# Optimization experiments

Hardware: AMD Instinct MI355X
Metric: run time of the kernel (lower is better)

## Reference

```python
import jax, jax.numpy as jnp
import numpy as np

B, NSEQ, SEQ_PER = 2, 4, 256
S = NSEQ * SEQ_PER            # total sequence (stocks interleaved along seq dim)
D, H, HD = 1024, 16, 64       # d_model, nhead, head_dim
HD2, HD4 = HD // 2, HD // 4
DFF = 4096
LAMBDA_INIT = 0.2             # lambda_init_fn(0) = 0.8 - 0.6*exp(0)
SCALING = 1.0 / float(np.sqrt(HD2))
EPS_DEF = float(np.finfo(np.float32).eps)   # torch RMSNorm default eps (eps=None)
EPS_ATTN = 1e-5


def _rms(x, w, eps):
    return x * jax.lax.rsqrt(jnp.mean(x * x, axis=-1, keepdims=True) + eps) * w


def _rope(x, fc):
    # x: (B, T, NSEQ, 2H, HD2); fc: (T, HD4, 2) holding (cos, sin)
    xr = x.reshape(x.shape[:-1] + (HD4, 2))
    c = fc[None, :, None, None, :, 0]
    s = fc[None, :, None, None, :, 1]
    x0, x1 = xr[..., 0], xr[..., 1]
    return jnp.stack([x0 * c - x1 * s, x0 * s + x1 * c], axis=-1).reshape(x.shape)


def setup_inputs():
    key = jax.random.key(0)
    ks = jax.random.split(key, 16)
    def w(i, shape, std=0.02):
        return jax.random.normal(ks[i], shape, jnp.float32) * std
    # true RoPE table for seq_per_stock-1 positions
    t = jnp.arange(SEQ_PER - 1, dtype=jnp.float32)[:, None]
    inv = 1.0 / (10000.0 ** (jnp.arange(HD4, dtype=jnp.float32) / HD4))
    ang = t * inv[None, :]
    return {
        "x": jax.random.normal(ks[0], (B, S, D), jnp.float32),
        "freqs_cis": jnp.stack([jnp.cos(ang), jnp.sin(ang)], axis=-1),
        "w_norm1": jnp.ones((D,), jnp.float32),
        "w_norm2": jnp.ones((D,), jnp.float32),
        "Wq": w(1, (H * HD, D)), "bq": jnp.zeros((H * HD,), jnp.float32),
        "Wk": w(2, (H * HD, D)), "bk": jnp.zeros((H * HD,), jnp.float32),
        "Wv": w(3, (H * HD, D)), "bv": jnp.zeros((H * HD,), jnp.float32),
        "Wo": w(4, (D, H * HD)), "bo": jnp.zeros((D,), jnp.float32),
        "lq1": w(5, (HD2,), 0.1), "lk1": w(6, (HD2,), 0.1),
        "lq2": w(7, (HD2,), 0.1), "lk2": w(8, (HD2,), 0.1),
        "w_attn_norm": jnp.ones((HD,), jnp.float32),
        "Wg": w(9, (2 * DFF, D)), "bg": jnp.zeros((2 * DFF,), jnp.float32),
        "Wout": w(10, (D, DFF)), "bout": jnp.zeros((D,), jnp.float32),
    }


def reference(x, freqs_cis, w_norm1, w_norm2, Wq, bq, Wk, bk, Wv, bv, Wo, bo,
              lq1, lk1, lq2, lk2, w_attn_norm, Wg, bg, Wout, bout):
    Bz, Sz, _ = x.shape
    h = _rms(x, w_norm1, EPS_DEF)
    q = (h @ Wq.T + bq).reshape(Bz, SEQ_PER, NSEQ, 2 * H, HD2)
    k = (h @ Wk.T + bk).reshape(Bz, SEQ_PER, NSEQ, 2 * H, HD2)
    v = (h @ Wv.T + bv).reshape(Bz, Sz, H, HD).transpose(0, 2, 1, 3)   # (B,H,S,HD), interleaved order
    # RoPE on all but the first per-stock timestep; same freqs for every stock
    q = jnp.concatenate([q[:, :1], _rope(q[:, 1:], freqs_cis)], axis=1)
    k = jnp.concatenate([k[:, :1], _rope(k[:, 1:], freqs_cis)], axis=1)
    # reorder q/k to stock-major flat sequence (torch permute(0,4,1,2,3)+reshape)
    q = q.transpose(0, 2, 1, 3, 4).reshape(Bz, Sz, 2 * H, HD2).transpose(0, 2, 1, 3)
    k = k.transpose(0, 2, 1, 3, 4).reshape(Bz, Sz, 2 * H, HD2).transpose(0, 2, 1, 3)
    scores = jnp.einsum('bhqd,bhkd->bhqk', q, k) * SCALING              # (B,2H,S,S)
    causal = jnp.triu(jnp.ones((SEQ_PER, SEQ_PER), bool), 1)
    mask = jnp.tile(causal, (NSEQ, NSEQ))   # block-tiled causal, as torch .repeat
    att = jnp.sign(scores) * jax.nn.softmax(
        jnp.where(mask, -1e30, jnp.abs(scores)), axis=-1)
    lam = jnp.exp(jnp.sum(lk1 * lq1)) - jnp.exp(jnp.sum(lk2 * lq2)) + LAMBDA_INIT
    att = att.reshape(Bz, H, 2, Sz, Sz)
    a1, a2 = att[:, :, 0], att[:, :, 1]
    G = jnp.mean(a1, axis=-2, keepdims=True)          # mean over queries, broadcast back
    a = jnp.where(mask, 0.0, a1 - lam * a2 + lam * G)
    ao = jnp.einsum('bhqk,bhkd->bhqd', a, v)          # v kept in interleaved order (faithful to source)
    ao = _rms(ao, w_attn_norm, EPS_ATTN)
    ao = ao.reshape(Bz, Sz, H * HD)  # flat reinterpret (B,H,S,HD)->(B,S,H*HD), matches torch reshape chain
    x = x + ao @ Wo.T + bo
    h2 = _rms(x, w_norm2, EPS_DEF)
    u, vg = jnp.split(h2 @ Wg.T + bg, 2, axis=-1)
    return x + (u * jax.nn.silu(vg)) @ Wout.T + bout
```

## Files before the change

kernel.cpp:

```cpp
#include <hip/hip_runtime.h>

#define LAMBDA_INIT 0.2f
#define SCALING 0.17677669529663687f
#define EPS_DEF 1.1920928955078125e-07f
#define EPS_ATTN 1e-5f

typedef unsigned short us4 __attribute__((ext_vector_type(4)));
typedef unsigned short us8v __attribute__((ext_vector_type(8)));
typedef float f32x4 __attribute__((ext_vector_type(4)));
typedef float f32x2 __attribute__((ext_vector_type(2)));
typedef __bf16 bf16x8 __attribute__((ext_vector_type(8)));

#define MFMA16(a, b, c) __builtin_amdgcn_mfma_f32_16x16x32_bf16((a), (b), (c), 0, 0, 0)

__device__ __forceinline__ float bf2f(unsigned short u) {
    unsigned int x = ((unsigned int)u) << 16;
    return __builtin_bit_cast(float, x);
}
__device__ __forceinline__ unsigned short f2bf(float f) {
    unsigned int x = __builtin_bit_cast(unsigned int, f);
    x += 0x7fffu + ((x >> 16) & 1u);
    return (unsigned short)(x >> 16);
}
__device__ __forceinline__ void split8(f32x4 a, f32x4 b, us8v& hi, us8v& lo) {
#pragma unroll
    for (int u = 0; u < 4; u++) {
        unsigned short h = f2bf(a[u]);
        hi[u] = h; lo[u] = f2bf(a[u] - bf2f(h));
        unsigned short h2 = f2bf(b[u]);
        hi[4 + u] = h2; lo[4 + u] = f2bf(b[u] - bf2f(h2));
    }
}
__device__ __forceinline__ bf16x8 ldb(const unsigned short* p) {
    return __builtin_bit_cast(bf16x8, *(const us8v*)p);
}

__device__ __forceinline__ float wave_sum(float v) {
#pragma unroll
    for (int o = 32; o > 0; o >>= 1) v += __shfl_down(v, o);
    return v;
}
__device__ __forceinline__ float block_sum(float v, float* red4) {
    int wv = threadIdx.x >> 6;
    float w = wave_sum(v);
    __syncthreads();
    if ((threadIdx.x & 63) == 0) red4[wv] = w;
    __syncthreads();
    return red4[0] + red4[1] + red4[2] + red4[3];
}

__global__ __launch_bounds__(256) void prep(float* __restrict__ G, float* __restrict__ lamp,
                                            const float* lq1, const float* lk1,
                                            const float* lq2, const float* lk2) {
    int i = (blockIdx.x * 256 + threadIdx.x) * 4;
    G[i] = 0.f; G[i + 1] = 0.f; G[i + 2] = 0.f; G[i + 3] = 0.f;
    if (blockIdx.x == 0 && threadIdx.x == 0) {
        float a = 0.f, c = 0.f;
        for (int d = 0; d < 32; d++) {
            a += lq1[d] * lk1[d];
            c += lq2[d] * lk2[d];
        }
        *lamp = expf(a) - expf(c) + LAMBDA_INIT;
    }
}

__global__ __launch_bounds__(256) void cvt_bf16(const float* __restrict__ s,
                                                unsigned short* __restrict__ d, int n4) {
    int i = blockIdx.x * 256 + threadIdx.x;
    if (i >= n4) return;
    f32x4 v = ((const f32x4*)s)[i];
    us4 o;
#pragma unroll
    for (int u = 0; u < 4; u++) o[u] = f2bf(v[u]);
    ((us4*)d)[i] = o;
}

__global__ __launch_bounds__(256) void cvt_split(const float* __restrict__ s,
                                                 unsigned short* __restrict__ hi,
                                                 unsigned short* __restrict__ lo, int n4) {
    int i = blockIdx.x * 256 + threadIdx.x;
    if (i >= n4) return;
    f32x4 v = ((const f32x4*)s)[i];
    us4 h, l;
#pragma unroll
    for (int u = 0; u < 4; u++) {
        h[u] = f2bf(v[u]);
        l[u] = f2bf(v[u] - bf2f(h[u]));
    }
    ((us4*)hi)[i] = h;
    ((us4*)lo)[i] = l;
}

template <int OUTBF>
__global__ __launch_bounds__(256) void rms_kernel(const float* __restrict__ x,
                                                  const float* __restrict__ w,
                                                  void* __restrict__ out, float eps) {
    int row = blockIdx.x;
    int tid = threadIdx.x;
    size_t base = (size_t)row * 1024 + tid * 4;
    f32x4 v = *(const f32x4*)(x + base);
    float ss = v[0]*v[0] + v[1]*v[1] + v[2]*v[2] + v[3]*v[3];
    __shared__ float red4[4];
    float tot = block_sum(ss, red4);
    float r = rsqrtf(tot * (1.0f / 1024.f) + eps);
    f32x4 wv = *(const f32x4*)(w + tid * 4);
    if (OUTBF) {
        us4 o;
#pragma unroll
        for (int i = 0; i < 4; i++) o[i] = f2bf(v[i] * r * wv[i]);
        *(us4*)((unsigned short*)out + base) = o;
    } else {
        f32x4 o;
#pragma unroll
        for (int i = 0; i < 4; i++) o[i] = v[i] * r * wv[i];
        *(f32x4*)((float*)out + base) = o;
    }
}

__global__ __launch_bounds__(256) void rms_split(const float* __restrict__ x,
                                                 const float* __restrict__ w,
                                                 unsigned short* __restrict__ hh,
                                                 unsigned short* __restrict__ hl, float eps) {
    int row = blockIdx.x;
    int tid = threadIdx.x;
    size_t base = (size_t)row * 1024 + tid * 4;
    f32x4 v = *(const f32x4*)(x + base);
    float ss = v[0]*v[0] + v[1]*v[1] + v[2]*v[2] + v[3]*v[3];
    __shared__ float red4[4];
    float tot = block_sum(ss, red4);
    float r = rsqrtf(tot * (1.0f / 1024.f) + eps);
    f32x4 wv = *(const f32x4*)(w + tid * 4);
    us4 oh, ol;
#pragma unroll
    for (int i = 0; i < 4; i++) {
        float val = v[i] * r * wv[i];
        oh[i] = f2bf(val);
        ol[i] = f2bf(val - bf2f(oh[i]));
    }
    *(us4*)(hh + base) = oh;
    *(us4*)(hl + base) = ol;
}

__global__ __launch_bounds__(256) void gemm_qkv_ps(
        const unsigned short* __restrict__ AH, const unsigned short* __restrict__ AL,
        const unsigned short* __restrict__ WqH, const unsigned short* __restrict__ WqL,
        const unsigned short* __restrict__ WkH, const unsigned short* __restrict__ WkL,
        const unsigned short* __restrict__ WvH, const unsigned short* __restrict__ WvL,
        const float* __restrict__ bq, const float* __restrict__ bk, const float* __restrict__ bv,
        float* __restrict__ Yq, float* __restrict__ Yk, float* __restrict__ Yv) {
    const int z = blockIdx.z;
    const unsigned short* BH = (z == 0) ? WqH : (z == 1) ? WkH : WvH;
    const unsigned short* BL = (z == 0) ? WqL : (z == 1) ? WkL : WvL;
    const float* bias = (z == 0) ? bq : (z == 1) ? bk : bv;
    float* out        = (z == 0) ? Yq : (z == 1) ? Yk : Yv;
    const int K = 1024, N = 1024;
    __shared__ __align__(16) unsigned short Ah[64][72];
    __shared__ __align__(16) unsigned short Al[64][72];
    __shared__ __align__(16) unsigned short Bh[64][72];
    __shared__ __align__(16) unsigned short Bl[64][72];
    const int t = threadIdx.x;
    const int bm = blockIdx.x, bn = blockIdx.y;
    const int lane = t & 63, w = t >> 6;
    const int wr = w >> 1, wc = w & 1;
    const int l15 = lane & 15, lg = lane >> 4;
    const int sr = t >> 2, sc = (t & 3) * 16;

    const unsigned short* AgH = AH + (size_t)(bm * 64 + sr) * K + sc;
    const unsigned short* AgL = AL + (size_t)(bm * 64 + sr) * K + sc;
    const unsigned short* BgH = BH + (size_t)(bn * 64 + sr) * K + sc;
    const unsigned short* BgL = BL + (size_t)(bn * 64 + sr) * K + sc;

    f32x4 acc[2][2] = {};

    us8v ah0 = *(const us8v*)AgH, ah1 = *(const us8v*)(AgH + 8);
    us8v al0 = *(const us8v*)AgL, al1 = *(const us8v*)(AgL + 8);
    us8v bh0 = *(const us8v*)BgH, bh1 = *(const us8v*)(BgH + 8);
    us8v bl0 = *(const us8v*)BgL, bl1 = *(const us8v*)(BgL + 8);

    for (int k0 = 0; k0 < K; k0 += 64) {
        __syncthreads();
        *(us8v*)&Ah[sr][sc] = ah0; *(us8v*)&Ah[sr][sc + 8] = ah1;
        *(us8v*)&Al[sr][sc] = al0; *(us8v*)&Al[sr][sc + 8] = al1;
        *(us8v*)&Bh[sr][sc] = bh0; *(us8v*)&Bh[sr][sc + 8] = bh1;
        *(us8v*)&Bl[sr][sc] = bl0; *(us8v*)&Bl[sr][sc + 8] = bl1;
        __syncthreads();
        if (k0 + 64 < K) {
            const int kn = k0 + 64;
            ah0 = *(const us8v*)(AgH + kn); ah1 = *(const us8v*)(AgH + kn + 8);
            al0 = *(const us8v*)(AgL + kn); al1 = *(const us8v*)(AgL + kn + 8);
            bh0 = *(const us8v*)(BgH + kn); bh1 = *(const us8v*)(BgH + kn + 8);
            bl0 = *(const us8v*)(BgL + kn); bl1 = *(const us8v*)(BgL + kn + 8);
        }
#pragma unroll
        for (int kk = 0; kk < 2; kk++) {
            bf16x8 afh[2], afl[2], bfh[2], bfl[2];
#pragma unroll
            for (int mi = 0; mi < 2; mi++) {
                afh[mi] = ldb(&Ah[wr * 32 + mi * 16 + l15][kk * 32 + lg * 8]);
                afl[mi] = ldb(&Al[wr * 32 + mi * 16 + l15][kk * 32 + lg * 8]);
            }
#pragma unroll
            for (int ni = 0; ni < 2; ni++) {
                bfh[ni] = ldb(&Bh[wc * 32 + ni * 16 + l15][kk * 32 + lg * 8]);
                bfl[ni] = ldb(&Bl[wc * 32 + ni * 16 + l15][kk * 32 + lg * 8]);
            }
#pragma unroll
            for (int mi = 0; mi < 2; mi++)
#pragma unroll
                for (int ni = 0; ni < 2; ni++) {
                    acc[mi][ni] = MFMA16(afl[mi], bfh[ni], acc[mi][ni]);
                    acc[mi][ni] = MFMA16(afh[mi], bfl[ni], acc[mi][ni]);
                    acc[mi][ni] = MFMA16(afh[mi], bfh[ni], acc[mi][ni]);
                }
        }
    }

    const int rbase = bm * 64 + wr * 32 + (lg << 2);
    const int cbase = bn * 64 + wc * 32 + l15;
#pragma unroll
    for (int mi = 0; mi < 2; mi++) {
#pragma unroll
        for (int ni = 0; ni < 2; ni++) {
            int col = cbase + ni * 16;
            float bb = bias[col];
#pragma unroll
            for (int r = 0; r < 4; r++) {
                int row = rbase + mi * 16 + r;
                out[(size_t)row * N + col] = acc[mi][ni][r] + bb;
            }
        }
    }
}

__global__ __launch_bounds__(256) void gemm_mfma_wb(const unsigned short* __restrict__ A,
                                                    const unsigned short* __restrict__ Bt,
                                                    const float* __restrict__ bias,
                                                    const float* __restrict__ res,
                                                    float* __restrict__ out,
                                                    int M, int N, int K) {
    __shared__ __align__(16) unsigned short As[64][72];
    __shared__ __align__(16) unsigned short Bs[64][72];
    const int t = threadIdx.x;
    const int bm = blockIdx.x, bn = blockIdx.y;
    const int lane = t & 63, w = t >> 6;
    const int wr = w >> 1, wc = w & 1;
    const int l15 = lane & 15, lg = lane >> 4;
    const int sr = t >> 2, sc = (t & 3) * 16;

    const unsigned short* Ag = A + (size_t)(bm * 64 + sr) * K + sc;
    const unsigned short* Bg = Bt + (size_t)(bn * 64 + sr) * K + sc;

    f32x4 acc[2][2] = {};

    us8v a0 = *(const us8v*)Ag, a1 = *(const us8v*)(Ag + 8);
    us8v b0 = *(const us8v*)Bg, b1 = *(const us8v*)(Bg + 8);

    for (int k0 = 0; k0 < K; k0 += 64) {
        __syncthreads();
        *(us8v*)&As[sr][sc]     = a0;
        *(us8v*)&As[sr][sc + 8] = a1;
        *(us8v*)&Bs[sr][sc]     = b0;
        *(us8v*)&Bs[sr][sc + 8] = b1;
        __syncthreads();
        if (k0 + 64 < K) {
            const int kn = k0 + 64;
            a0 = *(const us8v*)(Ag + kn); a1 = *(const us8v*)(Ag + kn + 8);
            b0 = *(const us8v*)(Bg + kn); b1 = *(const us8v*)(Bg + kn + 8);
        }
#pragma unroll
        for (int kk = 0; kk < 2; kk++) {
            bf16x8 af[2], bf[2];
#pragma unroll
            for (int mi = 0; mi < 2; mi++)
                af[mi] = ldb(&As[wr * 32 + mi * 16 + l15][kk * 32 + lg * 8]);
#pragma unroll
            for (int ni = 0; ni < 2; ni++)
                bf[ni] = ldb(&Bs[wc * 32 + ni * 16 + l15][kk * 32 + lg * 8]);
#pragma unroll
            for (int mi = 0; mi < 2; mi++)
#pragma unroll
                for (int ni = 0; ni < 2; ni++)
                    acc[mi][ni] = MFMA16(af[mi], bf[ni], acc[mi][ni]);
        }
    }

    const int rbase = bm * 64 + wr * 32 + (lg << 2);
    const int cbase = bn * 64 + wc * 32 + l15;
#pragma unroll
    for (int mi = 0; mi < 2; mi++) {
#pragma unroll
        for (int ni = 0; ni < 2; ni++) {
            int col = cbase + ni * 16;
            float bb = bias[col];
#pragma unroll
            for (int r = 0; r < 4; r++) {
                int row = rbase + mi * 16 + r;
                size_t oi = (size_t)row * N + col;
                out[oi] = acc[mi][ni][r] + bb + res[oi];
            }
        }
    }
}

__global__ __launch_bounds__(256) void gemm_gate_mfma(const unsigned short* __restrict__ A,
                                                      const float* __restrict__ Wg,
                                                      const float* __restrict__ bg,
                                                      unsigned short* __restrict__ mlp) {
    __shared__ __align__(16) unsigned short As[128][72];
    __shared__ __align__(16) unsigned short BsU[64][72];
    __shared__ __align__(16) unsigned short BsV[64][72];
    const int t = threadIdx.x;
    const int bm = blockIdx.x, bn = blockIdx.y;
    const int lane = t & 63, w = t >> 6;
    const int wr = w >> 1, wc = w & 1;
    const int l15 = lane & 15, lg = lane >> 4;
    const int sr = t >> 2, sc = (t & 3) * 16;

    const unsigned short* Ag  = A + (size_t)(bm * 128 + sr) * 1024 + sc;
    const unsigned short* Ag2 = Ag + (size_t)64 * 1024;
    const float* BgU = Wg + (size_t)(bn * 64 + sr) * 1024 + sc;
    const float* BgV = Wg + (size_t)(4096 + bn * 64 + sr) * 1024 + sc;

    f32x4 accU[4][2] = {};
    f32x4 accV[4][2] = {};

    for (int k0 = 0; k0 < 1024; k0 += 64) {
        us8v a0 = *(const us8v*)(Ag + k0);
        us8v a1 = *(const us8v*)(Ag + k0 + 8);
        us8v a2 = *(const us8v*)(Ag2 + k0);
        us8v a3 = *(const us8v*)(Ag2 + k0 + 8);
        f32x4 u0 = *(const f32x4*)(BgU + k0);
        f32x4 u1 = *(const f32x4*)(BgU + k0 + 4);
        f32x4 u2 = *(const f32x4*)(BgU + k0 + 8);
        f32x4 u3 = *(const f32x4*)(BgU + k0 + 12);
        f32x4 v0 = *(const f32x4*)(BgV + k0);
        f32x4 v1 = *(const f32x4*)(BgV + k0 + 4);
        f32x4 v2 = *(const f32x4*)(BgV + k0 + 8);
        f32x4 v3 = *(const f32x4*)(BgV + k0 + 12);
        us8v uw0, uw1, vw0, vw1;
#pragma unroll
        for (int u = 0; u < 4; u++) {
            uw0[u] = f2bf(u0[u]); uw0[4 + u] = f2bf(u1[u]);
            uw1[u] = f2bf(u2[u]); uw1[4 + u] = f2bf(u3[u]);
            vw0[u] = f2bf(v0[u]); vw0[4 + u] = f2bf(v1[u]);
            vw1[u] = f2bf(v2[u]); vw1[4 + u] = f2bf(v3[u]);
        }
        __syncthreads();
        *(us8v*)&As[sr][sc]          = a0;
        *(us8v*)&As[sr][sc + 8]      = a1;
        *(us8v*)&As[sr + 64][sc]     = a2;
        *(us8v*)&As[sr + 64][sc + 8] = a3;
        *(us8v*)&BsU[sr][sc]         = uw0;
        *(us8v*)&BsU[sr][sc + 8]     = uw1;
        *(us8v*)&BsV[sr][sc]         = vw0;
        *(us8v*)&BsV[sr][sc + 8]     = vw1;
        __syncthreads();
#pragma unroll
        for (int kk = 0; kk < 2; kk++) {
            bf16x8 af[4], bu[2], bv2[2];
#pragma unroll
            for (int mi = 0; mi < 4; mi++)
                af[mi] = ldb(&As[wr * 64 + mi * 16 + l15][kk * 32 + lg * 8]);
#pragma unroll
            for (int ni = 0; ni < 2; ni++) {
                bu[ni]  = ldb(&BsU[wc * 32 + ni * 16 + l15][kk * 32 + lg * 8]);
                bv2[ni] = ldb(&BsV[wc * 32 + ni * 16 + l15][kk * 32 + lg * 8]);
            }
#pragma unroll
            for (int mi = 0; mi < 4; mi++)
#pragma unroll
                for (int ni = 0; ni < 2; ni++) {
                    accU[mi][ni] = MFMA16(af[mi], bu[ni], accU[mi][ni]);
                    accV[mi][ni] = MFMA16(af[mi], bv2[ni], accV[mi][ni]);
                }
        }
    }

    const int rbase = bm * 128 + wr * 64 + (lg << 2);
    const int cbase = bn * 64 + wc * 32 + l15;
#pragma unroll
    for (int mi = 0; mi < 4; mi++) {
#pragma unroll
        for (int ni = 0; ni < 2; ni++) {
            int col = cbase + ni * 16;
            float bu_ = bg[col], bv_ = bg[4096 + col];
#pragma unroll
            for (int r = 0; r < 4; r++) {
                int row = rbase + mi * 16 + r;
                float u = accU[mi][ni][r] + bu_;
                float v = accV[mi][ni][r] + bv_;
                float s = v / (1.f + __expf(-v));
                mlp[(size_t)row * 4096 + col] = f2bf(u * s);
            }
        }
    }
}

__global__ __launch_bounds__(256) void rope_inplace(float* __restrict__ Y,
                                                    const float* __restrict__ fc) {
    int t = blockIdx.x;
    int s = t & 1023;
    int p = s >> 2;
    if (p == 0) return;
    int c0 = threadIdx.x * 4;
    float* y = Y + (size_t)t * 1024 + c0;
    int d4 = (c0 & 31) >> 1;
    f32x4 f = *(const f32x4*)(fc + ((size_t)(p - 1) * 16 + d4) * 2);
    float v0 = y[0], v1 = y[1], v2 = y[2], v3 = y[3];
    y[0] = v0 * f[0] - v1 * f[1];
    y[1] = v0 * f[1] + v1 * f[0];
    y[2] = v2 * f[2] - v3 * f[3];
    y[3] = v2 * f[3] + v3 * f[2];
}

__global__ __launch_bounds__(256) void rope_split_k(const float* __restrict__ Yk,
                                                    const float* __restrict__ fc,
                                                    unsigned short* __restrict__ KhG,
                                                    unsigned short* __restrict__ KlG) {
    int t = blockIdx.x;
    int s = t & 1023;
    int p = s >> 2;
    int c0 = threadIdx.x * 4;
    const float* y = Yk + (size_t)t * 1024 + c0;
    float v0 = y[0], v1 = y[1], v2 = y[2], v3 = y[3];
    if (p > 0) {
        int d4 = (c0 & 31) >> 1;
        f32x4 f = *(const f32x4*)(fc + ((size_t)(p - 1) * 16 + d4) * 2);
        float w0 = v0 * f[0] - v1 * f[1];
        float w1 = v0 * f[1] + v1 * f[0];
        float w2 = v2 * f[2] - v3 * f[3];
        float w3 = v2 * f[3] + v3 * f[2];
        v0 = w0; v1 = w1; v2 = w2; v3 = w3;
    }
    us4 hi, lo;
    hi[0] = f2bf(v0); lo[0] = f2bf(v0 - bf2f(hi[0]));
    hi[1] = f2bf(v1); lo[1] = f2bf(v1 - bf2f(hi[1]));
    hi[2] = f2bf(v2); lo[2] = f2bf(v2 - bf2f(hi[2]));
    hi[3] = f2bf(v3); lo[3] = f2bf(v3 - bf2f(hi[3]));
    *(us4*)(KhG + (size_t)t * 1024 + c0) = hi;
    *(us4*)(KlG + (size_t)t * 1024 + c0) = lo;
}

__global__ __launch_bounds__(256) void v_split_t(const float* __restrict__ Yv,
                                                 unsigned short* __restrict__ VtH,
                                                 unsigned short* __restrict__ VtL) {
    const int jc = blockIdx.x, h = blockIdx.y, b = blockIdx.z;
    __shared__ float tile[64][65];
    const int t = threadIdx.x;
    {
        const int jr = t >> 2, dc = (t & 3) * 16;
        const float* src = Yv + ((size_t)(b * 1024 + jc * 64 + jr) << 10) + h * 64 + dc;
        *(f32x4*)&tile[jr][dc]      = *(const f32x4*)src;
        *(f32x4*)&tile[jr][dc + 4]  = *(const f32x4*)(src + 4);
        *(f32x4*)&tile[jr][dc + 8]  = *(const f32x4*)(src + 8);
        *(f32x4*)&tile[jr][dc + 12] = *(const f32x4*)(src + 12);
    }
    __syncthreads();
    const int d = t >> 2, js = (t & 3) * 16;
    us8v h0, h1, l0, l1;
#pragma unroll
    for (int n = 0; n < 16; n++) {
        float val = tile[js + n][d];
        unsigned short hh = f2bf(val);
        unsigned short ll = f2bf(val - bf2f(hh));
        if (n < 8) { h0[n] = hh; l0[n] = ll; }
        else       { h1[n - 8] = hh; l1[n - 8] = ll; }
    }
    size_t ob = (((size_t)(b * 16 + h) * 64 + d) << 10) + jc * 64 + js;
    *(us8v*)(VtH + ob) = h0; *(us8v*)(VtH + ob + 8) = h1;
    *(us8v*)(VtL + ob) = l0; *(us8v*)(VtL + ob + 8) = l1;
}

__global__ __launch_bounds__(256) void pass_1(const float* __restrict__ Yq,
                                              const unsigned short* __restrict__ KhG,
                                              const unsigned short* __restrict__ KlG,
                                              const unsigned short* __restrict__ VtH,
                                              const unsigned short* __restrict__ VtL,
                                              const float* __restrict__ lamp,
                                              float* __restrict__ G,
                                              float* __restrict__ AOp) {
    const int blk = blockIdx.x;
    const int qc = 15 - (blk >> 5);
    const int h  = blk & 15;
    const int b  = (blk >> 4) & 1;
    const int t = threadIdx.x;
    const int lane = t & 63, w = t >> 6;
    const int l15 = lane & 15, lg = lane >> 4;

    __shared__ __align__(16) unsigned short Kh[64][72];
    __shared__ __align__(16) unsigned short Kl[64][72];
    __shared__ __align__(16) unsigned short Vth[64][72];
    __shared__ __align__(16) unsigned short Vtl[64][72];
    __shared__ __align__(16) unsigned short Wh[64][72];
    __shared__ __align__(16) unsigned short Wl[64][72];
    __shared__ float Gacc[1024];

    for (int i = t; i < 1024; i += 256) Gacc[i] = 0.f;

    us8v qh[2], ql[2];
    {
        const float* qp = Yq + ((size_t)(b * 1024 + qc * 64 + w * 16 + l15) << 10)
                          + h * 64 + lg * 8;
#pragma unroll
        for (int H = 0; H < 2; H++)
            split8(*(const f32x4*)(qp + H * 32), *(const f32x4*)(qp + H * 32 + 4), qh[H], ql[H]);
    }
    const int dq0 = w * 16 + (lg << 2);

    const int srow = t >> 2, ssub = t & 3;
    const int ptk = 4 * (srow & 15) + (srow >> 4);
    const unsigned short* KhB = KhG + ((size_t)(b * 1024) << 10) + h * 64;
    const unsigned short* KlB = KlG + ((size_t)(b * 1024) << 10) + h * 64;
    const unsigned short* VhB = VtH + (((size_t)(b * 16 + h) * 64 + srow) << 10) + ssub * 256;
    const unsigned short* VlB = VtL + (((size_t)(b * 16 + h) * 64 + srow) << 10) + ssub * 256;
    const float lam = *lamp;

    float z1r[4] = {0.f, 0.f, 0.f, 0.f};
    float z2r[4] = {0.f, 0.f, 0.f, 0.f};

    us8v rkh0, rkh1, rkl0, rkl1;
    {
        const unsigned short* kh = KhB + ((size_t)ptk << 10) + ssub * 16;
        const unsigned short* kl = KlB + ((size_t)ptk << 10) + ssub * 16;
        rkh0 = *(const us8v*)kh; rkh1 = *(const us8v*)(kh + 8);
        rkl0 = *(const us8v*)kl; rkl1 = *(const us8v*)(kl + 8);
    }
    for (int kc = 0; kc <= qc; kc++) {
        __syncthreads();
        *(us8v*)&Kh[srow][ssub * 16]     = rkh0;
        *(us8v*)&Kh[srow][ssub * 16 + 8] = rkh1;
        *(us8v*)&Kl[srow][ssub * 16]     = rkl0;
        *(us8v*)&Kl[srow][ssub * 16 + 8] = rkl1;
        __syncthreads();
        if (kc < qc) {
            const unsigned short* kh = KhB + ((size_t)((kc + 1) * 64 + ptk) << 10) + ssub * 16;
            const unsigned short* kl = KlB + ((size_t)((kc + 1) * 64 + ptk) << 10) + ssub * 16;
            rkh0 = *(const us8v*)kh; rkh1 = *(const us8v*)(kh + 8);
            rkl0 = *(const us8v*)kl; rkl1 = *(const us8v*)(kl + 8);
        }
        const int kpos = kc * 16 + l15;
#pragma unroll
        for (int kf = 0; kf < 4; kf++) {
            const int krow = kf * 16 + l15;
            const int kcol = lg * 8;
            bf16x8 b1h = ldb(&Kh[krow][kcol]),      b1l = ldb(&Kl[krow][kcol]);
            bf16x8 b2h = ldb(&Kh[krow][32 + kcol]), b2l = ldb(&Kl[krow][32 + kcol]);
            f32x4 s1 = {}, s2 = {};
            s1 = MFMA16(__builtin_bit_cast(bf16x8, ql[0]), b1h, s1);
            s1 = MFMA16(__builtin_bit_cast(bf16x8, qh[0]), b1l, s1);
            s1 = MFMA16(__builtin_bit_cast(bf16x8, qh[0]), b1h, s1);
            s2 = MFMA16(__builtin_bit_cast(bf16x8, ql[1]), b2h, s2);
            s2 = MFMA16(__builtin_bit_cast(bf16x8, qh[1]), b2l, s2);
            s2 = MFMA16(__builtin_bit_cast(bf16x8, qh[1]), b2h, s2);
#pragma unroll
            for (int r = 0; r < 4; r++) {
                int pq = (qc * 64 + dq0 + r) >> 2;
                if (kpos <= pq) {
                    z1r[r] += __expf(fabsf(s1[r] * SCALING));
                    z2r[r] += __expf(fabsf(s2[r] * SCALING));
                }
            }
        }
    }
#pragma unroll
    for (int r = 0; r < 4; r++) {
        float a = z1r[r];
        a += __shfl_xor(a, 1); a += __shfl_xor(a, 2);
        a += __shfl_xor(a, 4); a += __shfl_xor(a, 8);
        z1r[r] = 1.f / fmaxf(a, 1e-20f);
        float c = z2r[r];
        c += __shfl_xor(c, 1); c += __shfl_xor(c, 2);
        c += __shfl_xor(c, 4); c += __shfl_xor(c, 8);
        z2r[r] = 1.f / fmaxf(c, 1e-20f);
    }

    f32x4 ao[4] = {};

    us8v rvh0, rvh1, rvl0, rvl1;
    {
        const unsigned short* kh = KhB + ((size_t)ptk << 10) + ssub * 16;
        const unsigned short* kl = KlB + ((size_t)ptk << 10) + ssub * 16;
        rkh0 = *(const us8v*)kh; rkh1 = *(const us8v*)(kh + 8);
        rkl0 = *(const us8v*)kl; rkl1 = *(const us8v*)(kl + 8);
        rvh0 = *(const us8v*)VhB; rvh1 = *(const us8v*)(VhB + 8);
        rvl0 = *(const us8v*)VlB; rvl1 = *(const us8v*)(VlB + 8);
    }
    for (int kc = 0; kc <= qc; kc++) {
        __syncthreads();
        *(us8v*)&Kh[srow][ssub * 16]      = rkh0;
        *(us8v*)&Kh[srow][ssub * 16 + 8]  = rkh1;
        *(us8v*)&Kl[srow][ssub * 16]      = rkl0;
        *(us8v*)&Kl[srow][ssub * 16 + 8]  = rkl1;
        *(us8v*)&Vth[srow][ssub * 16]     = rvh0;
        *(us8v*)&Vth[srow][ssub * 16 + 8] = rvh1;
        *(us8v*)&Vtl[srow][ssub * 16]     = rvl0;
        *(us8v*)&Vtl[srow][ssub * 16 + 8] = rvl1;
        __syncthreads();
        if (kc < qc) {
            const unsigned short* kh = KhB + ((size_t)((kc + 1) * 64 + ptk) << 10) + ssub * 16;
            const unsigned short* kl = KlB + ((size_t)((kc + 1) * 64 + ptk) << 10) + ssub * 16;
            rkh0 = *(const us8v*)kh; rkh1 = *(const us8v*)(kh + 8);
            rkl0 = *(const us8v*)kl; rkl1 = *(const us8v*)(kl + 8);
            const unsigned short* vh = VhB + (kc + 1) * 16;
            const unsigned short* vl = VlB + (kc + 1) * 16;
            rvh0 = *(const us8v*)vh; rvh1 = *(const us8v*)(vh + 8);
            rvl0 = *(const us8v*)vl; rvl1 = *(const us8v*)(vl + 8);
        }
        const int kpos = kc * 16 + l15;
#pragma unroll
        for (int kf = 0; kf < 4; kf++) {
            const int krow = kf * 16 + l15;
            const int kcol = lg * 8;
            bf16x8 b1h = ldb(&Kh[krow][kcol]),      b1l = ldb(&Kl[krow][kcol]);
            bf16x8 b2h = ldb(&Kh[krow][32 + kcol]), b2l = ldb(&Kl[krow][32 + kcol]);
            f32x4 s1 = {}, s2 = {};
            s1 = MFMA16(__builtin_bit_cast(bf16x8, ql[0]), b1h, s1);
            s1 = MFMA16(__builtin_bit_cast(bf16x8, qh[0]), b1l, s1);
            s1 = MFMA16(__builtin_bit_cast(bf16x8, qh[0]), b1h, s1);
            s2 = MFMA16(__builtin_bit_cast(bf16x8, ql[1]), b2h, s2);
            s2 = MFMA16(__builtin_bit_cast(bf16x8, qh[1]), b2l, s2);
            s2 = MFMA16(__builtin_bit_cast(bf16x8, qh[1]), b2h, s2);
            const int kli = kf * 16 + l15;
            float colsum = 0.f;
#pragma unroll
            for (int r = 0; r < 4; r++) {
                int pq = (qc * 64 + dq0 + r) >> 2;
                float wv = 0.f, a1 = 0.f;
                if (kpos <= pq) {
                    float t1 = s1[r] * SCALING, t2 = s2[r] * SCALING;
                    float sg1 = (t1 > 0.f) ? 1.f : ((t1 < 0.f) ? -1.f : 0.f);
                    float sg2 = (t2 > 0.f) ? 1.f : ((t2 < 0.f) ? -1.f : 0.f);
                    a1 = sg1 * __expf(fabsf(t1)) * z1r[r];
                    wv = a1 - lam * (sg2 * __expf(fabsf(t2)) * z2r[r]);
                }
                colsum += a1;
                unsigned short hh = f2bf(wv);
                Wh[dq0 + r][kli] = hh;
                Wl[dq0 + r][kli] = f2bf(wv - bf2f(hh));
            }
            colsum += __shfl_xor(colsum, 16);
            colsum += __shfl_xor(colsum, 32);
            if (lane < 16) atomicAdd(&Gacc[kf * 256 + kc * 16 + lane], colsum);
        }
        __syncthreads();
#pragma unroll
        for (int kh2 = 0; kh2 < 2; kh2++) {
            bf16x8 wah = ldb(&Wh[w * 16 + l15][kh2 * 32 + lg * 8]);
            bf16x8 wal = ldb(&Wl[w * 16 + l15][kh2 * 32 + lg * 8]);
#pragma unroll
            for (int df = 0; df < 4; df++) {
                bf16x8 vbh = ldb(&Vth[df * 16 + l15][kh2 * 32 + lg * 8]);
                bf16x8 vbl = ldb(&Vtl[df * 16 + l15][kh2 * 32 + lg * 8]);
                ao[df] = MFMA16(wah, vbl, ao[df]);
                ao[df] = MFMA16(wal, vbh, ao[df]);
                ao[df] = MFMA16(wah, vbh, ao[df]);
            }
        }
    }

#pragma unroll
    for (int df = 0; df < 4; df++) {
#pragma unroll
        for (int r = 0; r < 4; r++) {
            int tq = qc * 64 + dq0 + r;
            int qrow = ((tq & 3) << 8) + (tq >> 2);
            AOp[((((size_t)(b * 16 + h)) << 10) + qrow) * 64 + df * 16 + l15] = ao[df][r];
        }
    }

    __syncthreads();
    float* Gb = G + ((size_t)(b * 16 + h) << 10);
    const int limp = (qc + 1) << 4;
    for (int idx = t; idx < 1024; idx += 256) {
        if ((idx & 255) < limp) atomicAdd(&Gb[idx], Gacc[idx]);
    }
}

__global__ __launch_bounds__(256) void pass_2a(const float* __restrict__ G,
                                               const float* __restrict__ Yv,
                                               float* __restrict__ GVpre) {
    const int h = blockIdx.x, b = blockIdx.y;
    const int t = threadIdx.x;
    __shared__ float Gl[1024];
    __shared__ float S[256][64];
    __shared__ float segsum[4][64];
    for (int i = t; i < 1024; i += 256) Gl[i] = G[((size_t)(b * 16 + h) << 10) + i];
    __syncthreads();
    const int d = t & 63, pg = t >> 6;
    const float* Yvb = Yv + ((size_t)b << 20) + h * 64 + d;
    for (int p0 = 0; p0 < 64; p0++) {
        int pos = pg * 64 + p0;
        float s = 0.f;
#pragma unroll
        for (int sq = 0; sq < 4; sq++) {
            int j = (sq << 8) + pos;
            s += Gl[j] * Yvb[(size_t)j << 10];
        }
        S[pos][d] = s;
    }
    __syncthreads();
    float acc = 0.f;
    for (int p0 = 0; p0 < 64; p0++) {
        int pos = pg * 64 + p0;
        acc += S[pos][d];
        S[pos][d] = acc;
    }
    segsum[pg][d] = acc;
    __syncthreads();
    float off = 0.f;
    for (int g = 0; g < pg; g++) off += segsum[g][d];
    float* gv = GVpre + (((size_t)(b * 16 + h)) << 14) + d;
    for (int p0 = 0; p0 < 64; p0++) {
        int pos = pg * 64 + p0;
        gv[pos << 6] = S[pos][d] + off;
    }
}

__global__ __launch_bounds__(256) void pass_2b(const float* __restrict__ AOp,
                                               const float* __restrict__ GVpre,
                                               const float* __restrict__ lamp,
                                               const float* __restrict__ wan,
                                               unsigned short* __restrict__ aoS) {
    const int qg = blockIdx.x;
    const int h = blockIdx.y, b = blockIdx.z;
    const int t = threadIdx.x;
    const int d = t & 63, rg = t >> 6;
    const float lamg = (*lamp) * (1.f / 1024.f);
    const float wv = wan[d];
    const float* aob = AOp + ((((size_t)(b * 16 + h)) << 10) + (qg << 8)) * 64 + d;
    const float* gvb = GVpre + (((size_t)(b * 16 + h)) << 14) + d;
    unsigned short* ob = aoS + ((size_t)b << 20) + ((size_t)h << 16) + ((size_t)(qg << 8) << 6) + d;
    for (int p0 = 0; p0 < 64; p0++) {
        int pq = p0 * 4 + rg;
        float ao = aob[(size_t)pq << 6] + lamg * gvb[(size_t)pq << 6];
        float ss = ao * ao;
#pragma unroll
        for (int o = 1; o < 64; o <<= 1) ss += __shfl_xor(ss, o);
        float rr_ = rsqrtf(ss * (1.f / 64.f) + EPS_ATTN);
        ob[(size_t)pq << 6] = f2bf(ao * rr_ * wv);
    }
}

extern "C" void kernel_launch(void* const* d_in, const int* in_sizes, int n_in,
                              void* d_out, int out_size, void* d_ws, size_t ws_size,
                              hipStream_t stream) {
    const float* x    = (const float*)d_in[0];
    const float* fc   = (const float*)d_in[1];
    const float* w1   = (const float*)d_in[2];
    const float* w2   = (const float*)d_in[3];
    const float* Wq   = (const float*)d_in[4];
    const float* bq   = (const float*)d_in[5];
    const float* Wk   = (const float*)d_in[6];
    const float* bk   = (const float*)d_in[7];
    const float* Wv   = (const float*)d_in[8];
    const float* bv   = (const float*)d_in[9];
    const float* Wo   = (const float*)d_in[10];
    const float* bo   = (const float*)d_in[11];
    const float* lq1  = (const float*)d_in[12];
    const float* lk1  = (const float*)d_in[13];
    const float* lq2  = (const float*)d_in[14];
    const float* lk2  = (const float*)d_in[15];
    const float* wan  = (const float*)d_in[16];
    const float* Wg   = (const float*)d_in[17];
    const float* bg   = (const float*)d_in[18];
    const float* Wout = (const float*)d_in[19];
    const float* bout = (const float*)d_in[20];

    char* ws = (char*)d_ws;
    const size_t MB = 1024 * 1024;
    float* G    = (float*)(ws);
    float* lam  = (float*)(ws + 256 * 1024);
    unsigned short* hH = (unsigned short*)(ws + 1 * MB);
    unsigned short* hL = (unsigned short*)(ws + 5 * MB);
    float* Yq   = (float*)(ws + 9 * MB);
    float* Yk   = (float*)(ws + 17 * MB);
    float* Yv   = (float*)(ws + 25 * MB);
    unsigned short* WqH = (unsigned short*)(ws + 33 * MB);
    unsigned short* WqL = (unsigned short*)(ws + 35 * MB);
    unsigned short* WkH = (unsigned short*)(ws + 37 * MB);
    unsigned short* WkL = (unsigned short*)(ws + 39 * MB);
    unsigned short* WvH = (unsigned short*)(ws + 41 * MB);
    unsigned short* WvL = (unsigned short*)(ws + 43 * MB);
    unsigned short* WoutB = (unsigned short*)(ws + 45 * MB);
    float* AOp  = (float*)(ws + 33 * MB);
    float* GVpre= (float*)(ws + 41 * MB);
    unsigned short* WoB = (unsigned short*)(ws + 43 * MB);
    unsigned short* KhG = (unsigned short*)(ws + 1 * MB);
    unsigned short* KlG = (unsigned short*)(ws + 5 * MB);
    unsigned short* VtH = (unsigned short*)(ws + 17 * MB);
    unsigned short* VtL = (unsigned short*)(ws + 21 * MB);
    unsigned short* aoS = (unsigned short*)(ws + 1 * MB);
    float* X1           = (float*)(ws + 9 * MB);
    unsigned short* h2b = (unsigned short*)(ws + 5 * MB);
    unsigned short* mlp = (unsigned short*)(ws + 17 * MB);

    prep<<<32, 256, 0, stream>>>(G, lam, lq1, lk1, lq2, lk2);
    cvt_bf16<<<4096, 256, 0, stream>>>(Wout, WoutB, 1048576);
    rms_split<<<2048, 256, 0, stream>>>(x, w1, hH, hL, EPS_DEF);
    cvt_split<<<1024, 256, 0, stream>>>(Wq, WqH, WqL, 262144);
    cvt_split<<<1024, 256, 0, stream>>>(Wk, WkH, WkL, 262144);
    cvt_split<<<1024, 256, 0, stream>>>(Wv, WvH, WvL, 262144);
    gemm_qkv_ps<<<dim3(32, 16, 3), 256, 0, stream>>>(hH, hL, WqH, WqL, WkH, WkL, WvH, WvL,
                                                     bq, bk, bv, Yq, Yk, Yv);
    cvt_bf16<<<1024, 256, 0, stream>>>(Wo, WoB, 262144);
    rope_inplace<<<2048, 256, 0, stream>>>(Yq, fc);
    rope_split_k<<<2048, 256, 0, stream>>>(Yk, fc, KhG, KlG);
    v_split_t<<<dim3(16, 16, 2), 256, 0, stream>>>(Yv, VtH, VtL);
    pass_1<<<512, 256, 0, stream>>>(Yq, KhG, KlG, VtH, VtL, lam, G, AOp);
    pass_2a<<<dim3(16, 2), 256, 0, stream>>>(G, Yv, GVpre);
    pass_2b<<<dim3(4, 16, 2), 256, 0, stream>>>(AOp, GVpre, lam, wan, aoS);
    dim3 gmf(32, 16);
    gemm_mfma_wb<<<gmf, 256, 0, stream>>>(aoS, WoB, bo, x, X1, 2048, 1024, 1024);
    rms_kernel<1><<<2048, 256, 0, stream>>>(X1, w2, h2b, EPS_DEF);
    gemm_gate_mfma<<<dim3(16, 64), 256, 0, stream>>>(h2b, Wg, bg, mlp);
    gemm_mfma_wb<<<gmf, 256, 0, stream>>>(mlp, WoutB, bout, X1, (float*)d_out, 2048, 1024, 4096);
}
```

Measured before the change: 439.2 us.

## Pre-convert gate weights to bf16, prefetch gate GEMM tiles, merge QKV weight splits

```diff
diff --git a/kernel.cpp b/kernel.cpp
--- a/kernel.cpp
+++ b/kernel.cpp
@@ -75,9 +75,15 @@
     ((us4*)d)[i] = o;
 }
 
-__global__ __launch_bounds__(256) void cvt_split(const float* __restrict__ s,
-                                                 unsigned short* __restrict__ hi,
-                                                 unsigned short* __restrict__ lo, int n4) {
+__global__ __launch_bounds__(256) void cvt_split3(
+        const float* __restrict__ s0, const float* __restrict__ s1, const float* __restrict__ s2,
+        unsigned short* __restrict__ h0, unsigned short* __restrict__ l0,
+        unsigned short* __restrict__ h1p, unsigned short* __restrict__ l1p,
+        unsigned short* __restrict__ h2p, unsigned short* __restrict__ l2p, int n4) {
+    const int z = blockIdx.y;
+    const float* s = (z == 0) ? s0 : (z == 1) ? s1 : s2;
+    unsigned short* hi = (z == 0) ? h0 : (z == 1) ? h1p : h2p;
+    unsigned short* lo = (z == 0) ? l0 : (z == 1) ? l1p : l2p;
     int i = blockIdx.x * 256 + threadIdx.x;
     if (i >= n4) return;
     f32x4 v = ((const f32x4*)s)[i];
@@ -302,10 +308,11 @@
     }
 }
 
-__global__ __launch_bounds__(256) void gemm_gate_mfma(const unsigned short* __restrict__ A,
-                                                      const float* __restrict__ Wg,
-                                                      const float* __restrict__ bg,
-                                                      unsigned short* __restrict__ mlp) {
+__global__ __launch_bounds__(256) void gemm_gate_wb(const unsigned short* __restrict__ A,
+                                                    const unsigned short* __restrict__ WuB,
+                                                    const unsigned short* __restrict__ WvB,
+                                                    const float* __restrict__ bg,
+                                                    unsigned short* __restrict__ mlp) {
     __shared__ __align__(16) unsigned short As[128][72];
     __shared__ __align__(16) unsigned short BsU[64][72];
     __shared__ __align__(16) unsigned short BsV[64][72];
@@ -318,43 +325,35 @@
 
     const unsigned short* Ag  = A + (size_t)(bm * 128 + sr) * 1024 + sc;
     const unsigned short* Ag2 = Ag + (size_t)64 * 1024;
-    const float* BgU = Wg + (size_t)(bn * 64 + sr) * 1024 + sc;
-    const float* BgV = Wg + (size_t)(4096 + bn * 64 + sr) * 1024 + sc;
+    const unsigned short* BgU = WuB + (size_t)(bn * 64 + sr) * 1024 + sc;
+    const unsigned short* BgV = WvB + (size_t)(bn * 64 + sr) * 1024 + sc;
 
     f32x4 accU[4][2] = {};
     f32x4 accV[4][2] = {};
 
+    us8v a0 = *(const us8v*)Ag,  a1 = *(const us8v*)(Ag + 8);
+    us8v a2 = *(const us8v*)Ag2, a3 = *(const us8v*)(Ag2 + 8);
+    us8v u0 = *(const us8v*)BgU, u1 = *(const us8v*)(BgU + 8);
+    us8v v0 = *(const us8v*)BgV, v1 = *(const us8v*)(BgV + 8);
+
     for (int k0 = 0; k0 < 1024; k0 += 64) {
-        us8v a0 = *(const us8v*)(Ag + k0);
-        us8v a1 = *(const us8v*)(Ag + k0 + 8);
-        us8v a2 = *(const us8v*)(Ag2 + k0);
-        us8v a3 = *(const us8v*)(Ag2 + k0 + 8);
-        f32x4 u0 = *(const f32x4*)(BgU + k0);
-        f32x4 u1 = *(const f32x4*)(BgU + k0 + 4);
-        f32x4 u2 = *(const f32x4*)(BgU + k0 + 8);
-        f32x4 u3 = *(const f32x4*)(BgU + k0 + 12);
-        f32x4 v0 = *(const f32x4*)(BgV + k0);
-        f32x4 v1 = *(const f32x4*)(BgV + k0 + 4);
-        f32x4 v2 = *(const f32x4*)(BgV + k0 + 8);
-        f32x4 v3 = *(const f32x4*)(BgV + k0 + 12);
-        us8v uw0, uw1, vw0, vw1;
-#pragma unroll
-        for (int u = 0; u < 4; u++) {
-            uw0[u] = f2bf(u0[u]); uw0[4 + u] = f2bf(u1[u]);
-            uw1[u] = f2bf(u2[u]); uw1[4 + u] = f2bf(u3[u]);
-            vw0[u] = f2bf(v0[u]); vw0[4 + u] = f2bf(v1[u]);
-            vw1[u] = f2bf(v2[u]); vw1[4 + u] = f2bf(v3[u]);
-        }
         __syncthreads();
         *(us8v*)&As[sr][sc]          = a0;
         *(us8v*)&As[sr][sc + 8]      = a1;
         *(us8v*)&As[sr + 64][sc]     = a2;
         *(us8v*)&As[sr + 64][sc + 8] = a3;
-        *(us8v*)&BsU[sr][sc]         = uw0;
-        *(us8v*)&BsU[sr][sc + 8]     = uw1;
-        *(us8v*)&BsV[sr][sc]         = vw0;
-        *(us8v*)&BsV[sr][sc + 8]     = vw1;
-        __syncthreads();
+        *(us8v*)&BsU[sr][sc]         = u0;
+        *(us8v*)&BsU[sr][sc + 8]     = u1;
+        *(us8v*)&BsV[sr][sc]         = v0;
+        *(us8v*)&BsV[sr][sc + 8]     = v1;
+        __syncthreads();
+        if (k0 + 64 < 1024) {
+            const int kn = k0 + 64;
+            a0 = *(const us8v*)(Ag + kn);  a1 = *(const us8v*)(Ag + kn + 8);
+            a2 = *(const us8v*)(Ag2 + kn); a3 = *(const us8v*)(Ag2 + kn + 8);
+            u0 = *(const us8v*)(BgU + kn); u1 = *(const us8v*)(BgU + kn + 8);
+            v0 = *(const us8v*)(BgV + kn); v1 = *(const us8v*)(BgV + kn + 8);
+        }
 #pragma unroll
         for (int kk = 0; kk < 2; kk++) {
             bf16x8 af[4], bu[2], bv2[2];
@@ -493,9 +492,9 @@
     __shared__ __align__(16) unsigned short Vtl[64][72];
     __shared__ __align__(16) unsigned short Wh[64][72];
     __shared__ __align__(16) unsigned short Wl[64][72];
-    __shared__ float Gacc[1024];
-
-    for (int i = t; i < 1024; i += 256) Gacc[i] = 0.f;
+    __shared__ float Gacc[4][1024];
+
+    for (int i = t; i < 4096; i += 256) ((float*)Gacc)[i] = 0.f;
 
     us8v qh[2], ql[2];
     {
@@ -640,9 +639,8 @@
             }
             colsum += __shfl_xor(colsum, 16);
             colsum += __shfl_xor(colsum, 32);
-            if (lane < 16) atomicAdd(&Gacc[kf * 256 + kc * 16 + lane], colsum);
-        }
-        __syncthreads();
+            if (lane < 16) Gacc[w][kf * 256 + kc * 16 + lane] = colsum;
+        }
 #pragma unroll
         for (int kh2 = 0; kh2 < 2; kh2++) {
             bf16x8 wah = ldb(&Wh[w * 16 + l15][kh2 * 32 + lg * 8]);
@@ -672,7 +670,10 @@
     float* Gb = G + ((size_t)(b * 16 + h) << 10);
     const int limp = (qc + 1) << 4;
     for (int idx = t; idx < 1024; idx += 256) {
-        if ((idx & 255) < limp) atomicAdd(&Gb[idx], Gacc[idx]);
+        if ((idx & 255) < limp) {
+            float s = Gacc[0][idx] + Gacc[1][idx] + Gacc[2][idx] + Gacc[3][idx];
+            atomicAdd(&Gb[idx], s);
+        }
     }
 }
 
@@ -781,7 +782,6 @@
     unsigned short* WkL = (unsigned short*)(ws + 39 * MB);
     unsigned short* WvH = (unsigned short*)(ws + 41 * MB);
     unsigned short* WvL = (unsigned short*)(ws + 43 * MB);
-    unsigned short* WoutB = (unsigned short*)(ws + 45 * MB);
     float* AOp  = (float*)(ws + 33 * MB);
     float* GVpre= (float*)(ws + 41 * MB);
     unsigned short* WoB = (unsigned short*)(ws + 43 * MB);
@@ -793,13 +793,13 @@
     float* X1           = (float*)(ws + 9 * MB);
     unsigned short* h2b = (unsigned short*)(ws + 5 * MB);
     unsigned short* mlp = (unsigned short*)(ws + 17 * MB);
+    unsigned short* WuB = (unsigned short*)(ws + 33 * MB);
+    unsigned short* WvB2= (unsigned short*)(ws + 41 * MB);
+    unsigned short* WoutB=(unsigned short*)(ws + 33 * MB);
 
     prep<<<32, 256, 0, stream>>>(G, lam, lq1, lk1, lq2, lk2);
-    cvt_bf16<<<4096, 256, 0, stream>>>(Wout, WoutB, 1048576);
     rms_split<<<2048, 256, 0, stream>>>(x, w1, hH, hL, EPS_DEF);
-    cvt_split<<<1024, 256, 0, stream>>>(Wq, WqH, WqL, 262144);
-    cvt_split<<<1024, 256, 0, stream>>>(Wk, WkH, WkL, 262144);
-    cvt_split<<<1024, 256, 0, stream>>>(Wv, WvH, WvL, 262144);
+    cvt_split3<<<dim3(1024, 3), 256, 0, stream>>>(Wq, Wk, Wv, WqH, WqL, WkH, WkL, WvH, WvL, 262144);
     gemm_qkv_ps<<<dim3(32, 16, 3), 256, 0, stream>>>(hH, hL, WqH, WqL, WkH, WkL, WvH, WvL,
                                                      bq, bk, bv, Yq, Yk, Yv);
     cvt_bf16<<<1024, 256, 0, stream>>>(Wo, WoB, 262144);
@@ -811,7 +811,10 @@
     pass_2b<<<dim3(4, 16, 2), 256, 0, stream>>>(AOp, GVpre, lam, wan, aoS);
     dim3 gmf(32, 16);
     gemm_mfma_wb<<<gmf, 256, 0, stream>>>(aoS, WoB, bo, x, X1, 2048, 1024, 1024);
+    cvt_bf16<<<4096, 256, 0, stream>>>(Wg, WuB, 1048576);
+    cvt_bf16<<<4096, 256, 0, stream>>>(Wg + 4194304, WvB2, 1048576);
     rms_kernel<1><<<2048, 256, 0, stream>>>(X1, w2, h2b, EPS_DEF);
-    gemm_gate_mfma<<<dim3(16, 64), 256, 0, stream>>>(h2b, Wg, bg, mlp);
+    gemm_gate_wb<<<dim3(16, 64), 256, 0, stream>>>(h2b, WuB, WvB2, bg, mlp);
+    cvt_bf16<<<4096, 256, 0, stream>>>(Wout, WoutB, 1048576);
     gemm_mfma_wb<<<gmf, 256, 0, stream>>>(mlp, WoutB, bout, X1, (float*)d_out, 2048, 1024, 4096);
 }
```

Measured after the change: 422.2 us. 1.04x faster.
